# Performance work log

Hardware: AMD Instinct MI355X
Metric: run time of the kernel (lower is better)

Reference implementation:

```python
import jax, jax.numpy as jnp
import numpy as np

TWO_PI = np.float32(2.0 * np.pi)
N_GABORS = 256
H = W = 512


def setup_inputs() -> dict:
    key = jax.random.key(0)
    ks = jax.random.split(key, 10)
    f32 = jnp.float32
    return {
        "grid_x": jax.random.uniform(ks[0], (H, W), dtype=f32),
        "grid_y": jax.random.uniform(ks[1], (H, W), dtype=f32),
        "u": jax.random.normal(ks[2], (N_GABORS,), dtype=f32),
        "v": jax.random.normal(ks[3], (N_GABORS,), dtype=f32),
        "theta": 2.0 * jax.random.normal(ks[4], (N_GABORS,), dtype=f32),
        "rel_sigma": 0.05 + 0.7 * jax.random.normal(ks[5], (N_GABORS,), dtype=f32),
        "rel_freq": 0.03 + 5.0 * jax.random.normal(ks[6], (N_GABORS,), dtype=f32),
        "gamma": 0.03 + 0.15 * jax.random.normal(ks[7], (N_GABORS,), dtype=f32),
        "psi": 3.0 * jax.random.normal(ks[8], (N_GABORS, 3), dtype=f32),
        "amplitude": 0.2 * jax.random.normal(ks[9], (N_GABORS, 3), dtype=f32),
    }


def reference(grid_x, grid_y, u, v, theta, rel_sigma, rel_freq, gamma, psi, amplitude):
    # Parameter range enforcement (enforce_parameter_ranges + forward clamps)
    uc = jnp.clip(u, -1.0, 1.0)
    vc = jnp.clip(v, -1.0, 1.0)
    th = jnp.clip(theta, -2.0, 2.0) * TWO_PI           # [N]
    sig = jnp.clip(rel_sigma, 1e-5, 5.0)               # [N]
    gam = jnp.clip(gamma, 1e-5, 5.0)                   # [N]
    psi_c = jnp.clip(psi, -1.0, 1.0)                   # [N,3]
    amp = jnp.clip(amplitude, 0.0, 1.0)                # [N,3]

    cr = jnp.cos(th)[:, None, None]
    sr = jnp.sin(th)[:, None, None]
    dx = grid_x[None, :, :] - uc[:, None, None]        # [N,H,W]
    dy = grid_y[None, :, :] - vc[:, None, None]
    x_rot = dx * cr + dy * sr                          # [N,H,W]
    y_rot = -dx * sr + dy * cr

    gaussian = jnp.exp(jnp.clip(
        -x_rot ** 2 / (2.0 * sig[:, None, None] ** 2)
        - y_rot ** 2 / (2.0 * gam[:, None, None] ** 2),
        -80.0, 80.0))                                  # [N,H,W]

    freq = TWO_PI / jnp.exp(rel_freq)                  # [N]
    phase = psi_c * TWO_PI                             # [N,3]
    fx = freq[:, None, None] * x_rot                   # [N,H,W]

    # cos(fx + phase) = cos(fx)cos(phase) - sin(fx)sin(phase):
    # contract the gabor dim without materializing [N,3,H,W].
    gc = gaussian * jnp.cos(fx)                        # [N,H,W]
    gs = gaussian * jnp.sin(fx)                        # [N,H,W]
    result = (jnp.einsum('nhw,nc->chw', gc, amp * jnp.cos(phase))
              - jnp.einsum('nhw,nc->chw', gs, amp * jnp.sin(phase)))  # [3,H,W]
    return jnp.clip(result, -1.0, 1.0)
```

## Files before the change

### kernel.cpp

```cpp
#include <hip/hip_runtime.h>
#include <stdint.h>

#define NG 256
#define HW (512*512)
#define NCELL 1024
#define CAP 384
#define SPILL_CAP 4096
#define PXB 4096
#define TWO_PI_F 6.283185307179586f
#define L2E 1.4426950408889634f
#define INV2PI_D 0.15915494309189535

static __device__ __forceinline__ float clampf(float x, float lo, float hi) {
    return fminf(fmaxf(x, lo), hi);
}

static __device__ __forceinline__ void compute_consts(
    int n,
    const float* __restrict__ u, const float* __restrict__ v,
    const float* __restrict__ theta, const float* __restrict__ rel_sigma,
    const float* __restrict__ rel_freq, const float* __restrict__ gamma,
    const float* __restrict__ psi, const float* __restrict__ amplitude,
    float4& A, float4& B, float4& C, float4& D)
{
    const float uc = clampf(u[n], -1.f, 1.f);
    const float vc = clampf(v[n], -1.f, 1.f);
    const float th = clampf(theta[n], -2.f, 2.f) * TWO_PI_F;
    const float sg = clampf(rel_sigma[n], 1e-5f, 5.f);
    const float gm = clampf(gamma[n], 1e-5f, 5.f);
    const float cr = (float)::cos((double)th);
    const float sr = (float)::sin((double)th);
    const float i2s = 1.0f / (2.0f * sg * sg);
    const float i2g = 1.0f / (2.0f * gm * gm);
    const float E  = (float)::exp((double)rel_freq[n]);
    const float fq = TWO_PI_F / E;
    A = make_float4(uc, vc, cr, sr);
    B = make_float4(-(i2s * L2E), -(i2g * L2E), fq, 0.f);
    float ac[3], as[3];
    #pragma unroll
    for (int c = 0; c < 3; ++c) {
        const float ph = clampf(psi[n*3 + c], -1.f, 1.f) * TWO_PI_F;
        const float a  = clampf(amplitude[n*3 + c], 0.f, 1.f);
        ac[c] = a * (float)::cos((double)ph);
        as[c] = a * (float)::sin((double)ph);
    }
    C = make_float4(ac[0], ac[1], ac[2], 0.f);
    D = make_float4(as[0], as[1], as[2], 0.f);
}

static __device__ __forceinline__ void accum_list(
    const float4* __restrict__ base, int ngab,
    float gx, float gy, float& a0, float& a1, float& a2)
{
    const float c1f = 0.15915494309189535f;
    const float c2f = (float)(INV2PI_D - (double)0.15915494309189535f);
    for (int j = 0; j < ngab; ++j) {
        const float4 k0 = base[j];
        const float4 k1 = base[NG + j];
        const float dx = gx - k0.x;
        const float dy = gy - k0.y;
        float xr, yr;
        {
            #pragma clang fp contract(off)
            xr = dx * k0.z + dy * k0.w;
            yr = dy * k0.z - dx * k0.w;
        }
        const float e2 = fmaf(yr * yr, k1.y, xr * xr * k1.x);
        if (e2 > -20.0f) {
            const float g = __builtin_amdgcn_exp2f(e2);
            float fx;
            {
                #pragma clang fp contract(off)
                fx = k1.z * xr;
            }
            const float r1 = fx * c1f;
            const float nn = __builtin_rintf(r1);
            float t = __builtin_fmaf(fx, c1f, -nn);
            t = __builtin_fmaf(fx, c2f, t);
            const float s = __builtin_amdgcn_sinf(t);
            const float c = __builtin_amdgcn_cosf(t);
            const float4 k2 = base[2*NG + j];
            const float4 k3 = base[3*NG + j];
            a0 = fmaf(g, fmaf(-s, k3.x, c * k2.x), a0);
            a1 = fmaf(g, fmaf(-s, k3.y, c * k2.y), a1);
            a2 = fmaf(g, fmaf(-s, k3.z, c * k2.z), a2);
        }
    }
}

__global__ __launch_bounds__(256) void gabor_prep(
    const float* __restrict__ u, const float* __restrict__ v,
    const float* __restrict__ theta, const float* __restrict__ rel_sigma,
    const float* __restrict__ rel_freq, const float* __restrict__ gamma,
    const float* __restrict__ psi, const float* __restrict__ amplitude,
    float4* __restrict__ wconsts, int* __restrict__ counts,
    int* __restrict__ spilln)
{
    const int n = threadIdx.x;
    float4 A, B, C, D;
    compute_consts(n, u, v, theta, rel_sigma, rel_freq, gamma, psi, amplitude,
                   A, B, C, D);
    wconsts[n] = A; wconsts[NG+n] = B; wconsts[2*NG+n] = C; wconsts[3*NG+n] = D;
    counts[n] = 0; counts[256+n] = 0; counts[512+n] = 0; counts[768+n] = 0;
    if (n == 0) *spilln = 0;
}

__global__ __launch_bounds__(256) void gabor_cull(
    const float4* __restrict__ consts, uint8_t* __restrict__ glist,
    int* __restrict__ gcnt)
{
    const int b = blockIdx.x;
    const int tid = threadIdx.x;
    const float4 A = consts[tid];
    const float4 B = consts[NG + tid];
    const float4 C = consts[2*NG + tid];
    const float4 D = consts[3*NG + tid];
    const float cxc = ((b & 31) + 0.5f) * 0.03125f;
    const float cyc = ((b >> 5) + 0.5f) * 0.03125f;
    const float dx = cxc - A.x, dy = cyc - A.y;
    const float xrc = dx * A.z + dy * A.w;
    const float yrc = dy * A.z - dx * A.w;
    const float R = 0.0222f;
    const float xl = fmaxf(fabsf(xrc) - R, 0.f);
    const float yl = fmaxf(fabsf(yrc) - R, 0.f);
    const float e2max = xl*xl*B.x + yl*yl*B.y;
    const bool nz = (C.x != 0.f) | (C.y != 0.f) | (C.z != 0.f) |
                    (D.x != 0.f) | (D.y != 0.f) | (D.z != 0.f);
    const bool act = (e2max > -20.0f) && nz;

    __shared__ int wbase[4];
    const unsigned long long m = __ballot(act);
    const int lane = tid & 63, w = tid >> 6;
    if (lane == 0) wbase[w] = __popcll(m);
    __syncthreads();
    int base = 0;
    for (int i = 0; i < w; ++i) base += wbase[i];
    if (act) {
        const int pos = base + __popcll(m & ((1ull << lane) - 1ull));
        glist[b*NG + pos] = (uint8_t)tid;
    }
    if (tid == 0) gcnt[b] = wbase[0] + wbase[1] + wbase[2] + wbase[3];
}

__global__ __launch_bounds__(256) void gabor_bin(
    const float* __restrict__ grid_x, const float* __restrict__ grid_y,
    int* __restrict__ counts, int* __restrict__ bucket,
    int* __restrict__ spill, int* __restrict__ spilln)
{
    __shared__ int hist[NCELL];
    __shared__ int base[NCELL];
    const int tid = threadIdx.x;
    #pragma unroll
    for (int i = 0; i < NCELL/256; ++i) hist[i*256 + tid] = 0;
    __syncthreads();

    uint32_t rec[PXB/256];
    const int p0 = blockIdx.x * PXB;
    #pragma unroll
    for (int i = 0; i < PXB/256; ++i) {
        const int p = p0 + i*256 + tid;
        const float x = grid_x[p], y = grid_y[p];
        int ix = (int)(x * 32.0f); ix = min(max(ix, 0), 31);
        int iy = (int)(y * 32.0f); iy = min(max(iy, 0), 31);
        const int cell = iy*32 + ix;
        const int lr = atomicAdd(&hist[cell], 1);
        rec[i] = ((uint32_t)cell << 13) | (uint32_t)lr;
    }
    __syncthreads();
    #pragma unroll
    for (int i = 0; i < NCELL/256; ++i) {
        const int c = i*256 + tid;
        const int h = hist[c];
        base[c] = (h > 0) ? atomicAdd(&counts[c], h) : 0;
    }
    __syncthreads();
    #pragma unroll
    for (int i = 0; i < PXB/256; ++i) {
        const int p = p0 + i*256 + tid;
        const int cell = (int)(rec[i] >> 13);
        const int g = base[cell] + (int)(rec[i] & 0x1FFFu);
        if (g < CAP) bucket[cell*CAP + g] = p;
        else { const int t2 = atomicAdd(spilln, 1); if (t2 < SPILL_CAP) spill[t2] = p; }
    }
}

__global__ __launch_bounds__(128) void gabor_render(
    const float4* __restrict__ consts, const uint8_t* __restrict__ glist,
    const int* __restrict__ gcnt, const int* __restrict__ counts,
    const int* __restrict__ bucket, const int* __restrict__ spill,
    const int* __restrict__ spilln,
    const float* __restrict__ grid_x, const float* __restrict__ grid_y,
    float* __restrict__ out)
{
    __shared__ float4 cs[4 * NG];
    const int cell = blockIdx.x >> 1, par = blockIdx.x & 1;
    const int tid = threadIdx.x;
    const int ng = gcnt[cell];
    for (int j = tid; j < ng; j += 128) {
        const int n = glist[cell*NG + j];
        cs[j]        = consts[n];
        cs[NG + j]   = consts[NG + n];
        cs[2*NG + j] = consts[2*NG + n];
        cs[3*NG + j] = consts[3*NG + n];
    }
    __syncthreads();
    const int cnt = min(counts[cell], CAP);
    for (int i = par*128 + tid; i < cnt; i += 256) {
        const int p = bucket[cell*CAP + i];
        const float gx = grid_x[p], gy = grid_y[p];
        float a0 = 0.f, a1 = 0.f, a2 = 0.f;
        accum_list(cs, ng, gx, gy, a0, a1, a2);
        out[p]        = clampf(a0, -1.f, 1.f);
        out[HW + p]   = clampf(a1, -1.f, 1.f);
        out[2*HW + p] = clampf(a2, -1.f, 1.f);
    }
    if (blockIdx.x == 0) {
        const int sc = min(*spilln, SPILL_CAP);
        for (int i = tid; i < sc; i += 128) {
            const int p = spill[i];
            const float gx = grid_x[p], gy = grid_y[p];
            float a0 = 0.f, a1 = 0.f, a2 = 0.f;
            accum_list(consts, NG, gx, gy, a0, a1, a2);
            out[p]        = clampf(a0, -1.f, 1.f);
            out[HW + p]   = clampf(a1, -1.f, 1.f);
            out[2*HW + p] = clampf(a2, -1.f, 1.f);
        }
    }
}

__global__ __launch_bounds__(256) void gabor_consts_kernel(
    const float* __restrict__ u, const float* __restrict__ v,
    const float* __restrict__ theta, const float* __restrict__ rel_sigma,
    const float* __restrict__ rel_freq, const float* __restrict__ gamma,
    const float* __restrict__ psi, const float* __restrict__ amplitude,
    float4* __restrict__ ws)
{
    const int n = threadIdx.x;
    float4 A, B, C, D;
    compute_consts(n, u, v, theta, rel_sigma, rel_freq, gamma, psi, amplitude,
                   A, B, C, D);
    ws[n] = A; ws[NG + n] = B; ws[2*NG + n] = C; ws[3*NG + n] = D;
}

__global__ __launch_bounds__(256) void gabor_fwd_ws(
    const float4* __restrict__ ws,
    const float* __restrict__ grid_x, const float* __restrict__ grid_y,
    float* __restrict__ out)
{
    __shared__ float4 cs[4 * NG];
    const int tid = threadIdx.x;
    cs[tid]        = ws[tid];
    cs[tid + NG]   = ws[tid + NG];
    cs[tid + 2*NG] = ws[tid + 2*NG];
    cs[tid + 3*NG] = ws[tid + 3*NG];
    __syncthreads();
    const int p = blockIdx.x * 256 + tid;
    const float gx = grid_x[p], gy = grid_y[p];
    float a0 = 0.f, a1 = 0.f, a2 = 0.f;
    accum_list(cs, NG, gx, gy, a0, a1, a2);
    out[p]        = clampf(a0, -1.f, 1.f);
    out[HW + p]   = clampf(a1, -1.f, 1.f);
    out[2*HW + p] = clampf(a2, -1.f, 1.f);
}

__global__ __launch_bounds__(256) void gabor_fwd_fused(
    const float* __restrict__ grid_x, const float* __restrict__ grid_y,
    const float* __restrict__ u, const float* __restrict__ v,
    const float* __restrict__ theta, const float* __restrict__ rel_sigma,
    const float* __restrict__ rel_freq, const float* __restrict__ gamma,
    const float* __restrict__ psi, const float* __restrict__ amplitude,
    float* __restrict__ out)
{
    __shared__ float4 cs[4 * NG];
    const int tid = threadIdx.x;
    {
        float4 A, B, C, D;
        compute_consts(tid, u, v, theta, rel_sigma, rel_freq, gamma, psi,
                       amplitude, A, B, C, D);
        cs[tid] = A; cs[tid + NG] = B; cs[tid + 2*NG] = C; cs[tid + 3*NG] = D;
    }
    __syncthreads();
    const int p = blockIdx.x * 256 + tid;
    const float gx = grid_x[p], gy = grid_y[p];
    float a0 = 0.f, a1 = 0.f, a2 = 0.f;
    accum_list(cs, NG, gx, gy, a0, a1, a2);
    out[p]        = clampf(a0, -1.f, 1.f);
    out[HW + p]   = clampf(a1, -1.f, 1.f);
    out[2*HW + p] = clampf(a2, -1.f, 1.f);
}

extern "C" void kernel_launch(void* const* d_in, const int* in_sizes, int n_in,
                              void* d_out, int out_size, void* d_ws, size_t ws_size,
                              hipStream_t stream) {
    const float* grid_x    = (const float*)d_in[0];
    const float* grid_y    = (const float*)d_in[1];
    const float* u         = (const float*)d_in[2];
    const float* v         = (const float*)d_in[3];
    const float* theta     = (const float*)d_in[4];
    const float* rel_sigma = (const float*)d_in[5];
    const float* rel_freq  = (const float*)d_in[6];
    const float* gamma     = (const float*)d_in[7];
    const float* psi       = (const float*)d_in[8];
    const float* amplitude = (const float*)d_in[9];
    float* out = (float*)d_out;

    const size_t OFF_CONSTS = 0;
    const size_t OFF_COUNTS = 16384;
    const size_t OFF_GCNT   = 20480;
    const size_t OFF_SPN    = 24576;
    const size_t OFF_GLIST  = 24832;
    const size_t OFF_BUCKET = 286976;
    const size_t OFF_SPILL  = 1859840;
    const size_t NEED       = 1876224;

    char* w = (char*)d_ws;

    if (ws_size >= NEED) {
        float4*  consts = (float4*)(w + OFF_CONSTS);
        int*     counts = (int*)(w + OFF_COUNTS);
        int*     gcnt   = (int*)(w + OFF_GCNT);
        int*     spn    = (int*)(w + OFF_SPN);
        uint8_t* glist  = (uint8_t*)(w + OFF_GLIST);
        int*     bucket = (int*)(w + OFF_BUCKET);
        int*     spill  = (int*)(w + OFF_SPILL);

        gabor_prep<<<1, 256, 0, stream>>>(
            u, v, theta, rel_sigma, rel_freq, gamma, psi, amplitude,
            consts, counts, spn);
        gabor_cull<<<NCELL, 256, 0, stream>>>(consts, glist, gcnt);
        gabor_bin<<<HW / PXB, 256, 0, stream>>>(
            grid_x, grid_y, counts, bucket, spill, spn);
        gabor_render<<<2*NCELL, 128, 0, stream>>>(
            consts, glist, gcnt, counts, bucket, spill, spn,
            grid_x, grid_y, out);
    } else if (ws_size >= 4u * NG * sizeof(float4)) {
        float4* ws = (float4*)d_ws;
        gabor_consts_kernel<<<1, NG, 0, stream>>>(
            u, v, theta, rel_sigma, rel_freq, gamma, psi, amplitude, ws);
        gabor_fwd_ws<<<HW / 256, 256, 0, stream>>>(ws, grid_x, grid_y, out);
    } else {
        gabor_fwd_fused<<<HW / 256, 256, 0, stream>>>(
            grid_x, grid_y, u, v, theta, rel_sigma, rel_freq, gamma,
            psi, amplitude, out);
    }
}
```

Baseline: 38.20 us.

## Fuse culling into render, merge prep with binning, two pixels per thread

Replaces four launches with a memset plus two kernels. Gabor constants are now computed by an extra block of the binning kernel, and the per-cell culling moves into the render kernel, so the glist/gcnt buffers are gone. Binning also stores each pixel's coordinates contiguously per cell, removing the gathered grid reads at render time. Render uses one block per cell with each thread handling two pixels, which reuses each shared-memory constant load across both pixels at the cost of more registers and divergence when only one pixel passes the cutoff. Each render block now redoes the cull over all 256 gabors.

```diff
diff --git a/kernel.cpp b/kernel.cpp
--- a/kernel.cpp
+++ b/kernel.cpp
@@ -73,83 +73,42 @@
                 #pragma clang fp contract(off)
                 fx = k1.z * xr;
             }
-            const float r1 = fx * c1f;
-            const float nn = __builtin_rintf(r1);
+            const float nn = __builtin_rintf(fx * c1f);
             float t = __builtin_fmaf(fx, c1f, -nn);
             t = __builtin_fmaf(fx, c2f, t);
             const float s = __builtin_amdgcn_sinf(t);
             const float c = __builtin_amdgcn_cosf(t);
             const float4 k2 = base[2*NG + j];
             const float4 k3 = base[3*NG + j];
-            a0 = fmaf(g, fmaf(-s, k3.x, c * k2.x), a0);
-            a1 = fmaf(g, fmaf(-s, k3.y, c * k2.y), a1);
-            a2 = fmaf(g, fmaf(-s, k3.z, c * k2.z), a2);
-        }
-    }
-}
-
-__global__ __launch_bounds__(256) void gabor_prep(
+            const float gc = g * c, gs = g * s;
+            a0 = fmaf(gc, k2.x, fmaf(-gs, k3.x, a0));
+            a1 = fmaf(gc, k2.y, fmaf(-gs, k3.y, a1));
+            a2 = fmaf(gc, k2.z, fmaf(-gs, k3.z, a2));
+        }
+    }
+}
+
+__global__ __launch_bounds__(256) void gabor_bin_consts(
+    const float* __restrict__ grid_x, const float* __restrict__ grid_y,
     const float* __restrict__ u, const float* __restrict__ v,
     const float* __restrict__ theta, const float* __restrict__ rel_sigma,
     const float* __restrict__ rel_freq, const float* __restrict__ gamma,
     const float* __restrict__ psi, const float* __restrict__ amplitude,
-    float4* __restrict__ wconsts, int* __restrict__ counts,
-    int* __restrict__ spilln)
-{
-    const int n = threadIdx.x;
-    float4 A, B, C, D;
-    compute_consts(n, u, v, theta, rel_sigma, rel_freq, gamma, psi, amplitude,
-                   A, B, C, D);
-    wconsts[n] = A; wconsts[NG+n] = B; wconsts[2*NG+n] = C; wconsts[3*NG+n] = D;
-    counts[n] = 0; counts[256+n] = 0; counts[512+n] = 0; counts[768+n] = 0;
-    if (n == 0) *spilln = 0;
-}
-
-__global__ __launch_bounds__(256) void gabor_cull(
-    const float4* __restrict__ consts, uint8_t* __restrict__ glist,
-    int* __restrict__ gcnt)
-{
-    const int b = blockIdx.x;
+    float4* __restrict__ consts, int* __restrict__ counts,
+    int* __restrict__ bucket, float2* __restrict__ bxy,
+    int* __restrict__ spill, int* __restrict__ spilln)
+{
     const int tid = threadIdx.x;
-    const float4 A = consts[tid];
-    const float4 B = consts[NG + tid];
-    const float4 C = consts[2*NG + tid];
-    const float4 D = consts[3*NG + tid];
-    const float cxc = ((b & 31) + 0.5f) * 0.03125f;
-    const float cyc = ((b >> 5) + 0.5f) * 0.03125f;
-    const float dx = cxc - A.x, dy = cyc - A.y;
-    const float xrc = dx * A.z + dy * A.w;
-    const float yrc = dy * A.z - dx * A.w;
-    const float R = 0.0222f;
-    const float xl = fmaxf(fabsf(xrc) - R, 0.f);
-    const float yl = fmaxf(fabsf(yrc) - R, 0.f);
-    const float e2max = xl*xl*B.x + yl*yl*B.y;
-    const bool nz = (C.x != 0.f) | (C.y != 0.f) | (C.z != 0.f) |
-                    (D.x != 0.f) | (D.y != 0.f) | (D.z != 0.f);
-    const bool act = (e2max > -20.0f) && nz;
-
-    __shared__ int wbase[4];
-    const unsigned long long m = __ballot(act);
-    const int lane = tid & 63, w = tid >> 6;
-    if (lane == 0) wbase[w] = __popcll(m);
-    __syncthreads();
-    int base = 0;
-    for (int i = 0; i < w; ++i) base += wbase[i];
-    if (act) {
-        const int pos = base + __popcll(m & ((1ull << lane) - 1ull));
-        glist[b*NG + pos] = (uint8_t)tid;
-    }
-    if (tid == 0) gcnt[b] = wbase[0] + wbase[1] + wbase[2] + wbase[3];
-}
-
-__global__ __launch_bounds__(256) void gabor_bin(
-    const float* __restrict__ grid_x, const float* __restrict__ grid_y,
-    int* __restrict__ counts, int* __restrict__ bucket,
-    int* __restrict__ spill, int* __restrict__ spilln)
-{
+    if (blockIdx.x == 64) {
+        float4 A, B, C, D;
+        compute_consts(tid, u, v, theta, rel_sigma, rel_freq, gamma, psi,
+                       amplitude, A, B, C, D);
+        consts[tid] = A; consts[NG+tid] = B;
+        consts[2*NG+tid] = C; consts[3*NG+tid] = D;
+        return;
+    }
     __shared__ int hist[NCELL];
     __shared__ int base[NCELL];
-    const int tid = threadIdx.x;
     #pragma unroll
     for (int i = 0; i < NCELL/256; ++i) hist[i*256 + tid] = 0;
     __syncthreads();
@@ -179,42 +138,132 @@
         const int p = p0 + i*256 + tid;
         const int cell = (int)(rec[i] >> 13);
         const int g = base[cell] + (int)(rec[i] & 0x1FFFu);
-        if (g < CAP) bucket[cell*CAP + g] = p;
-        else { const int t2 = atomicAdd(spilln, 1); if (t2 < SPILL_CAP) spill[t2] = p; }
+        if (g < CAP) {
+            bucket[cell*CAP + g] = p;
+            bxy[cell*CAP + g] = make_float2(grid_x[p], grid_y[p]);
+        } else {
+            const int t2 = atomicAdd(spilln, 1);
+            if (t2 < SPILL_CAP) spill[t2] = p;
+        }
     }
 }
 
 __global__ __launch_bounds__(128) void gabor_render(
-    const float4* __restrict__ consts, const uint8_t* __restrict__ glist,
-    const int* __restrict__ gcnt, const int* __restrict__ counts,
-    const int* __restrict__ bucket, const int* __restrict__ spill,
-    const int* __restrict__ spilln,
+    const float4* __restrict__ consts, const int* __restrict__ counts,
+    const int* __restrict__ bucket, const float2* __restrict__ bxy,
+    const int* __restrict__ spill, const int* __restrict__ spilln,
     const float* __restrict__ grid_x, const float* __restrict__ grid_y,
     float* __restrict__ out)
 {
     __shared__ float4 cs[4 * NG];
-    const int cell = blockIdx.x >> 1, par = blockIdx.x & 1;
+    __shared__ int s_wb[2];
+    const int cell = blockIdx.x;
     const int tid = threadIdx.x;
-    const int ng = gcnt[cell];
-    for (int j = tid; j < ng; j += 128) {
-        const int n = glist[cell*NG + j];
-        cs[j]        = consts[n];
-        cs[NG + j]   = consts[NG + n];
-        cs[2*NG + j] = consts[2*NG + n];
-        cs[3*NG + j] = consts[3*NG + n];
-    }
-    __syncthreads();
+    const float cxc = ((cell & 31) + 0.5f) * 0.03125f;
+    const float cyc = ((cell >> 5) + 0.5f) * 0.03125f;
+
+    int total = 0;
+    #pragma unroll
+    for (int r = 0; r < 2; ++r) {
+        const int g = r*128 + tid;
+        const float4 A = consts[g];
+        const float4 B = consts[NG + g];
+        const float4 C = consts[2*NG + g];
+        const float4 D = consts[3*NG + g];
+        const float dx = cxc - A.x, dy = cyc - A.y;
+        const float xrc = dx * A.z + dy * A.w;
+        const float yrc = dy * A.z - dx * A.w;
+        const float R = 0.0222f;
+        const float xl = fmaxf(fabsf(xrc) - R, 0.f);
+        const float yl = fmaxf(fabsf(yrc) - R, 0.f);
+        const float e2max = xl*xl*B.x + yl*yl*B.y;
+        const bool nz = (C.x != 0.f) | (C.y != 0.f) | (C.z != 0.f) |
+                        (D.x != 0.f) | (D.y != 0.f) | (D.z != 0.f);
+        const bool act = (e2max > -20.0f) && nz;
+        const unsigned long long m = __ballot(act);
+        const int lane = tid & 63, w = tid >> 6;
+        if (lane == 0) s_wb[w] = __popcll(m);
+        __syncthreads();
+        const int pos = total + (w ? s_wb[0] : 0)
+                      + __popcll(m & ((1ull << lane) - 1ull));
+        if (act) { cs[pos] = A; cs[NG+pos] = B; cs[2*NG+pos] = C; cs[3*NG+pos] = D; }
+        total += s_wb[0] + s_wb[1];
+        __syncthreads();
+    }
+    const int ng = total;
+
+    const float c1f = 0.15915494309189535f;
+    const float c2f = (float)(INV2PI_D - (double)0.15915494309189535f);
     const int cnt = min(counts[cell], CAP);
-    for (int i = par*128 + tid; i < cnt; i += 256) {
-        const int p = bucket[cell*CAP + i];
-        const float gx = grid_x[p], gy = grid_y[p];
-        float a0 = 0.f, a1 = 0.f, a2 = 0.f;
-        accum_list(cs, ng, gx, gy, a0, a1, a2);
-        out[p]        = clampf(a0, -1.f, 1.f);
-        out[HW + p]   = clampf(a1, -1.f, 1.f);
-        out[2*HW + p] = clampf(a2, -1.f, 1.f);
-    }
-    if (blockIdx.x == 0) {
+    const int sb = cell * CAP;
+    for (int b0 = 0; b0 < cnt; b0 += 256) {
+        const int i0 = b0 + 2*tid;
+        if (i0 >= cnt) continue;
+        const int i1 = i0 + 1;
+        const bool v1 = i1 < cnt;
+        const float2 xy0 = bxy[sb + i0];
+        const float2 xy1 = v1 ? bxy[sb + i1] : xy0;
+        float p00 = 0.f, p01 = 0.f, p02 = 0.f;
+        float p10 = 0.f, p11 = 0.f, p12 = 0.f;
+        for (int j = 0; j < ng; ++j) {
+            const float4 k0 = cs[j];
+            const float4 k1 = cs[NG + j];
+            const float dx0 = xy0.x - k0.x, dy0 = xy0.y - k0.y;
+            const float dx1 = xy1.x - k0.x, dy1 = xy1.y - k0.y;
+            float xr0, yr0, xr1, yr1;
+            {
+                #pragma clang fp contract(off)
+                xr0 = dx0 * k0.z + dy0 * k0.w;
+                yr0 = dy0 * k0.z - dx0 * k0.w;
+                xr1 = dx1 * k0.z + dy1 * k0.w;
+                yr1 = dy1 * k0.z - dx1 * k0.w;
+            }
+            const float e20 = fmaf(yr0*yr0, k1.y, xr0*xr0 * k1.x);
+            const float e21 = fmaf(yr1*yr1, k1.y, xr1*xr1 * k1.x);
+            if (e20 > -20.0f || e21 > -20.0f) {
+                const float g0 = __builtin_amdgcn_exp2f(e20);
+                const float g1 = __builtin_amdgcn_exp2f(e21);
+                float fx0, fx1;
+                {
+                    #pragma clang fp contract(off)
+                    fx0 = k1.z * xr0;
+                    fx1 = k1.z * xr1;
+                }
+                const float n0 = __builtin_rintf(fx0 * c1f);
+                const float n1 = __builtin_rintf(fx1 * c1f);
+                float t0 = __builtin_fmaf(fx0, c1f, -n0);
+                float t1 = __builtin_fmaf(fx1, c1f, -n1);
+                t0 = __builtin_fmaf(fx0, c2f, t0);
+                t1 = __builtin_fmaf(fx1, c2f, t1);
+                const float s0 = __builtin_amdgcn_sinf(t0);
+                const float c0 = __builtin_amdgcn_cosf(t0);
+                const float s1 = __builtin_amdgcn_sinf(t1);
+                const float c1 = __builtin_amdgcn_cosf(t1);
+                const float4 k2 = cs[2*NG + j];
+                const float4 k3 = cs[3*NG + j];
+                const float gc0 = g0*c0, gs0 = g0*s0;
+                const float gc1 = g1*c1, gs1 = g1*s1;
+                p00 = fmaf(gc0, k2.x, fmaf(-gs0, k3.x, p00));
+                p01 = fmaf(gc0, k2.y, fmaf(-gs0, k3.y, p01));
+                p02 = fmaf(gc0, k2.z, fmaf(-gs0, k3.z, p02));
+                p10 = fmaf(gc1, k2.x, fmaf(-gs1, k3.x, p10));
+                p11 = fmaf(gc1, k2.y, fmaf(-gs1, k3.y, p11));
+                p12 = fmaf(gc1, k2.z, fmaf(-gs1, k3.z, p12));
+            }
+        }
+        const int p0 = bucket[sb + i0];
+        out[p0]        = clampf(p00, -1.f, 1.f);
+        out[HW + p0]   = clampf(p01, -1.f, 1.f);
+        out[2*HW + p0] = clampf(p02, -1.f, 1.f);
+        if (v1) {
+            const int p1 = bucket[sb + i1];
+            out[p1]        = clampf(p10, -1.f, 1.f);
+            out[HW + p1]   = clampf(p11, -1.f, 1.f);
+            out[2*HW + p1] = clampf(p12, -1.f, 1.f);
+        }
+    }
+
+    if (cell == 0) {
         const int sc = min(*spilln, SPILL_CAP);
         for (int i = tid; i < sc; i += 128) {
             const int p = spill[i];
@@ -306,33 +355,28 @@
 
     const size_t OFF_CONSTS = 0;
     const size_t OFF_COUNTS = 16384;
-    const size_t OFF_GCNT   = 20480;
-    const size_t OFF_SPN    = 24576;
-    const size_t OFF_GLIST  = 24832;
-    const size_t OFF_BUCKET = 286976;
-    const size_t OFF_SPILL  = 1859840;
-    const size_t NEED       = 1876224;
+    const size_t OFF_SPN    = 20480;
+    const size_t OFF_SPILL  = 20736;
+    const size_t OFF_BUCKET = 37120;
+    const size_t OFF_BXY    = 1609984;
+    const size_t NEED       = 4755712;
 
     char* w = (char*)d_ws;
 
     if (ws_size >= NEED) {
-        float4*  consts = (float4*)(w + OFF_CONSTS);
-        int*     counts = (int*)(w + OFF_COUNTS);
-        int*     gcnt   = (int*)(w + OFF_GCNT);
-        int*     spn    = (int*)(w + OFF_SPN);
-        uint8_t* glist  = (uint8_t*)(w + OFF_GLIST);
-        int*     bucket = (int*)(w + OFF_BUCKET);
-        int*     spill  = (int*)(w + OFF_SPILL);
-
-        gabor_prep<<<1, 256, 0, stream>>>(
-            u, v, theta, rel_sigma, rel_freq, gamma, psi, amplitude,
-            consts, counts, spn);
-        gabor_cull<<<NCELL, 256, 0, stream>>>(consts, glist, gcnt);
-        gabor_bin<<<HW / PXB, 256, 0, stream>>>(
-            grid_x, grid_y, counts, bucket, spill, spn);
-        gabor_render<<<2*NCELL, 128, 0, stream>>>(
-            consts, glist, gcnt, counts, bucket, spill, spn,
-            grid_x, grid_y, out);
+        float4* consts = (float4*)(w + OFF_CONSTS);
+        int*    counts = (int*)(w + OFF_COUNTS);
+        int*    spn    = (int*)(w + OFF_SPN);
+        int*    spill  = (int*)(w + OFF_SPILL);
+        int*    bucket = (int*)(w + OFF_BUCKET);
+        float2* bxy    = (float2*)(w + OFF_BXY);
+
+        hipMemsetAsync(w + OFF_COUNTS, 0, 4096 + 256, stream);
+        gabor_bin_consts<<<65, 256, 0, stream>>>(
+            grid_x, grid_y, u, v, theta, rel_sigma, rel_freq, gamma,
+            psi, amplitude, consts, counts, bucket, bxy, spill, spn);
+        gabor_render<<<NCELL, 128, 0, stream>>>(
+            consts, counts, bucket, bxy, spill, spn, grid_x, grid_y, out);
     } else if (ws_size >= 4u * NG * sizeof(float4)) {
         float4* ws = (float4*)d_ws;
         gabor_consts_kernel<<<1, NG, 0, stream>>>(
```

New measurement: 46.47 us. 1.22x slower.
